# Performance work log

Measured on AMD Instinct MI355X. Metric: run time of the kernel, lower is better.

Reference implementation:

```python
import jax, jax.numpy as jnp
import numpy as np

HEADS = 8
DEPTH = 2
LN_EPS = 1e-5


def _layernorm(x, g, b):
    m = jnp.mean(x, axis=-1, keepdims=True)
    v = jnp.var(x, axis=-1, keepdims=True)
    return (x - m) / jnp.sqrt(v + LN_EPS) * g + b


def setup_inputs() -> dict:
    key = jax.random.key(0)
    ks = jax.random.split(key, 16)
    b, c, n, t = 4, 64, 512, 12
    L, H = DEPTH, 256  # depth, mlp_dim
    s = 0.05
    return {
        'x': jax.random.normal(ks[0], (b, c, n, t), jnp.float32),
        'adj': jax.random.uniform(ks[1], (n, n), jnp.float32) / n,
        'pos': 0.02 * jax.random.normal(ks[2], (1, n, c), jnp.float32),
        'qkv_w': s * jax.random.normal(ks[3], (L, 3 * c, c), jnp.float32),
        'proj_w': s * jax.random.normal(ks[4], (L, c, c), jnp.float32),
        'proj_b': jnp.zeros((L, c), jnp.float32),
        'ln_g': jnp.ones((L, c), jnp.float32),
        'ln_b': jnp.zeros((L, c), jnp.float32),
        'ff_w1': s * jax.random.normal(ks[5], (L, H, c), jnp.float32),
        'ff_b1': jnp.zeros((L, H), jnp.float32),
        'ff_w2': s * jax.random.normal(ks[6], (L, c, H), jnp.float32),
        'ff_b2': jnp.zeros((L, c), jnp.float32),
        'gcn_w': s * jax.random.normal(ks[7], (L, c, 3 * c), jnp.float32),  # Conv2d 1x1: [c_out, 3*c_in]
        'gcn_b': jnp.zeros((L, c), jnp.float32),
    }


def reference(x, adj, pos, qkv_w, proj_w, proj_b, ln_g, ln_b,
              ff_w1, ff_b1, ff_w2, ff_b2, gcn_w, gcn_b):
    b, c, n, t = x.shape
    hd = c // HEADS
    scale = hd ** (-0.5)
    # [b, c, n, t] -> [b*t, n, c]
    h = jnp.transpose(x, (0, 3, 2, 1)).reshape(b * t, n, c) + pos
    for l in range(DEPTH):
        residual = h.reshape(b, t, n, c)
        # --- manual MHA (no pre-norm around attention, faithful to source) ---
        qkv = jnp.einsum('bnc,oc->bno', h, qkv_w[l])  # [bt, n, 3c]
        qkv = qkv.reshape(b * t, n, 3, HEADS, hd).transpose(2, 0, 3, 1, 4)
        q, k, v = qkv[0], qkv[1], qkv[2]  # [bt, heads, n, hd]
        attn = jax.nn.softmax(jnp.einsum('bhnd,bhmd->bhnm', q, k) * scale, axis=-1)
        o = jnp.einsum('bhnm,bhmd->bhnd', attn, v)
        o = o.transpose(0, 2, 1, 3).reshape(b * t, n, c)
        o = jnp.einsum('bnc,oc->bno', o, proj_w[l]) + proj_b[l]
        h = o + h
        # --- PreNorm FeedForward ---
        y = _layernorm(h, ln_g[l], ln_b[l])
        y = jax.nn.gelu(jnp.einsum('bnc,hc->bnh', y, ff_w1[l]) + ff_b1[l], approximate=False)
        y = jnp.einsum('bnh,ch->bnc', y, ff_w2[l]) + ff_b2[l]
        h = y + h
        # --- GCN on residual (order=2 diffusion) ---
        r = jnp.transpose(residual, (0, 3, 2, 1))  # [b, c, n, t]
        x1 = jnp.einsum('bcvt,vw->bcwt', r, adj)
        x2 = jnp.einsum('bcvt,vw->bcwt', x1, adj)
        cat = jnp.concatenate([r, x1, x2], axis=1)  # [b, 3c, n, t]
        g = jnp.einsum('bknt,ok->bont', cat, gcn_w[l]) + gcn_b[l][None, :, None, None]
        h = jnp.transpose(g, (0, 3, 2, 1)).reshape(b * t, n, c) + h
    return jnp.transpose(h.reshape(b, t, n, c), (0, 3, 2, 1))
```

## Files before the change

### kernel.cpp

```cpp
#include <hip/hip_runtime.h>
#include <math.h>


typedef __fp16 half_t;
typedef __attribute__((ext_vector_type(2))) __fp16 half2v;
typedef __attribute__((ext_vector_type(4))) __fp16 half4v;
typedef __attribute__((ext_vector_type(4))) float f32x4;

union PU  { half2v h2[2]; half4v h4; };
union F4H { float4 f; half4v h[2]; };
union F2H { float2 f2; half4v h4; };

#define ATS 72
#define BTS 68
#define KLS 20
#define QLS 20
#define VTS 516

__global__ __launch_bounds__(256) void k_pre(const float* __restrict__ x,
                                             const float* __restrict__ pos,
                                             const float* __restrict__ adj,
                                             const float* __restrict__ qkv_w,
                                             const float* __restrict__ proj_w,
                                             const float* __restrict__ ff_w1,
                                             const float* __restrict__ ff_w2,
                                             const float* __restrict__ gcn_w,
                                             float* __restrict__ h,
                                             half_t* __restrict__ hh,
                                             half_t* __restrict__ adjTh,
                                             half_t* __restrict__ wh,
                                             half_t* __restrict__ adjT2h) {
    __shared__ __align__(16) char smem[17920];
    float* t = (float*)smem;
    int tid = threadIdx.x;
    int bidx = blockIdx.x;
    if (bidx < 384) {
        int b = bidx / 96, vt0 = (bidx % 96) * 64;
#pragma unroll
        for (int i = 0; i < 4; ++i) {
            int g = tid + i * 256;
            int r = g >> 4, q = g & 15;
            *(float4*)&t[r * 65 + 4 * q] =
                *(const float4*)(x + ((size_t)(b * 64 + r)) * 6144 + vt0 + 4 * q);
        }
        __syncthreads();
#pragma unroll
        for (int i = 0; i < 4; ++i) {
            int g = tid + i * 256;
            int r = g >> 4, q = g & 15;
            int vt = vt0 + r;
            int v = vt / 12, tt = vt - v * 12;
            float4 pv = *(const float4*)(pos + v * 64 + 4 * q);
            float4 o;
            o.x = t[(4 * q + 0) * 65 + r] + pv.x;
            o.y = t[(4 * q + 1) * 65 + r] + pv.y;
            o.z = t[(4 * q + 2) * 65 + r] + pv.z;
            o.w = t[(4 * q + 3) * 65 + r] + pv.w;
            size_t idx = ((size_t)((b * 12 + tt) * 512 + v)) * 64 + 4 * q;
            *(float4*)(h + idx) = o;
            PU u;
            u.h2[0] = __builtin_amdgcn_cvt_pkrtz(o.x, o.y);
            u.h2[1] = __builtin_amdgcn_cvt_pkrtz(o.z, o.w);
            *(half4v*)(hh + idx) = u.h4;
        }
    } else if (bidx < 448) {
        int fb = bidx - 384;
        int v0 = (fb & 7) * 64, w0 = (fb >> 3) * 64;
#pragma unroll
        for (int i = 0; i < 4; ++i) {
            int g = tid + i * 256;
            int r = g >> 4, q = g & 15;
            float4 a = *(const float4*)(adj + (size_t)(v0 + r) * 512 + w0 + 4 * q);
            t[(4 * q + 0) * 65 + r] = a.x;
            t[(4 * q + 1) * 65 + r] = a.y;
            t[(4 * q + 2) * 65 + r] = a.z;
            t[(4 * q + 3) * 65 + r] = a.w;
        }
        __syncthreads();
#pragma unroll
        for (int i = 0; i < 4; ++i) {
            int g = tid + i * 256;
            int rw = g >> 4, q = g & 15;
            const float* src = &t[rw * 65 + 4 * q];
            PU u;
            u.h2[0] = __builtin_amdgcn_cvt_pkrtz(src[0], src[1]);
            u.h2[1] = __builtin_amdgcn_cvt_pkrtz(src[2], src[3]);
            *(half4v*)(adjTh + (size_t)(w0 + rw) * 512 + v0 + 4 * q) = u.h4;
        }
    } else if (bidx < 568) {
        int i = ((bidx - 448) * 256 + tid) * 4;
        float4 v;
        if (i < 24576) v = *(const float4*)(qkv_w + i);
        else if (i < 32768) v = *(const float4*)(proj_w + (i - 24576));
        else if (i < 65536) v = *(const float4*)(ff_w1 + (i - 32768));
        else if (i < 98304) v = *(const float4*)(ff_w2 + (i - 65536));
        else v = *(const float4*)(gcn_w + (i - 98304));
        PU u;
        u.h2[0] = __builtin_amdgcn_cvt_pkrtz(v.x, v.y);
        u.h2[1] = __builtin_amdgcn_cvt_pkrtz(v.z, v.w);
        *(half4v*)(wh + i) = u.h4;
    } else {
        half_t* a_t = (half_t*)smem;
        half_t* b_t = (half_t*)smem + 64 * ATS;
        int fb = bidx - 568;
        int w0 = (fb & 7) * 64, v0 = (fb >> 3) * 64;
        int wave = tid >> 6, lane = tid & 63;
        int lm = lane & 15, lg = lane >> 4;
        const f32x4 zc = {0.f, 0.f, 0.f, 0.f};
        f32x4 acc[4] = {zc, zc, zc, zc};
        for (int kc = 0; kc < 8; ++kc) {
#pragma unroll
            for (int i = 0; i < 4; ++i) {
                int g = tid + i * 256;
                int uu = g >> 4, q = g & 15;
                float4 a = *(const float4*)(adj + (size_t)(kc * 64 + uu) * 512 + w0 + 4 * q);
                a_t[(4 * q + 0) * ATS + uu] = (half_t)a.x;
                a_t[(4 * q + 1) * ATS + uu] = (half_t)a.y;
                a_t[(4 * q + 2) * ATS + uu] = (half_t)a.z;
                a_t[(4 * q + 3) * ATS + uu] = (half_t)a.w;
            }
#pragma unroll
            for (int i = 0; i < 4; ++i) {
                int g = tid + i * 256;
                int c = g >> 4, q = g & 15;
                float4 a = *(const float4*)(adj + (size_t)(v0 + c) * 512 + kc * 64 + 4 * q);
                PU u;
                u.h2[0] = __builtin_amdgcn_cvt_pkrtz(a.x, a.y);
                u.h2[1] = __builtin_amdgcn_cvt_pkrtz(a.z, a.w);
                *(half4v*)&b_t[c * BTS + 4 * q] = u.h4;
            }
            __syncthreads();
#pragma unroll
            for (int k16 = 0; k16 < 4; ++k16) {
                half4v af = *(const half4v*)&a_t[(wave * 16 + lm) * ATS + k16 * 16 + lg * 4];
#pragma unroll
                for (int nt = 0; nt < 4; ++nt) {
                    half4v bf = *(const half4v*)&b_t[(nt * 16 + lm) * BTS + k16 * 16 + lg * 4];
                    acc[nt] = __builtin_amdgcn_mfma_f32_16x16x16f16(af, bf, acc[nt], 0, 0, 0);
                }
            }
            __syncthreads();
        }
#pragma unroll
        for (int nt = 0; nt < 4; ++nt)
#pragma unroll
            for (int r = 0; r < 4; ++r)
                adjT2h[(size_t)(w0 + wave * 16 + lg * 4 + r) * 512 + v0 + nt * 16 + lm] =
                    (half_t)acc[nt][r];
    }
}

__global__ __launch_bounds__(256) void k_qd(const half_t* __restrict__ hh,
                                            const half_t* __restrict__ Wh,
                                            half_t* __restrict__ qh,
                                            half_t* __restrict__ kh,
                                            half_t* __restrict__ vh,
                                            const half_t* __restrict__ adjTh,
                                            const half_t* __restrict__ adjT2h,
                                            half_t* __restrict__ x1h,
                                            half_t* __restrict__ x2h) {
    __shared__ __align__(16) half_t sbuf[2 * 64 * ATS + 64 * BTS];
    int tid = threadIdx.x;
    int bidx = blockIdx.x;
    int wave = tid >> 6, lane = tid & 63;
    int lm = lane & 15, lg = lane >> 4;
    const f32x4 zc = {0.f, 0.f, 0.f, 0.f};

    if (bidx < 384) {
        int wid = bidx * 4 + wave;
        int row = wid * 16 + lm;
        half4v xf[4];
#pragma unroll
        for (int kc = 0; kc < 4; ++kc) {
            F2H u;
            u.f2 = *(const float2*)(hh + (size_t)row * 64 + kc * 16 + lg * 4);
            xf[kc] = u.h4;
        }
        const float SC = 0.35355339059327373f * 1.4426950408889634f;
        int bt = row >> 9, v = row & 511;
        half4v wf[4];
#pragma unroll
        for (int kc = 0; kc < 4; ++kc)
            wf[kc] = *(const half4v*)(Wh + (size_t)lm * 64 + kc * 16 + lg * 4);
#pragma unroll
        for (int nt = 0; nt < 12; ++nt) {
            half4v cw[4];
#pragma unroll
            for (int kc = 0; kc < 4; ++kc) cw[kc] = wf[kc];
            if (nt < 11) {
#pragma unroll
                for (int kc = 0; kc < 4; ++kc)
                    wf[kc] = *(const half4v*)(Wh + (size_t)((nt + 1) * 16 + lm) * 64 + kc * 16 + lg * 4);
            }
            f32x4 acc = zc;
#pragma unroll
            for (int kc = 0; kc < 4; ++kc)
                acc = __builtin_amdgcn_mfma_f32_16x16x16f16(cw[kc], xf[kc], acc, 0, 0, 0);
            int s = nt >> 2;
            if (s == 0) { acc[0] *= SC; acc[1] *= SC; acc[2] *= SC; acc[3] *= SC; }
            int head = ((nt & 3) << 1) + (lg >> 1);
            int d0 = (lg & 1) * 4;
            PU o2;
            o2.h2[0] = __builtin_amdgcn_cvt_pkrtz(acc[0], acc[1]);
            o2.h2[1] = __builtin_amdgcn_cvt_pkrtz(acc[2], acc[3]);
            half_t* dst = (s == 0) ? qh : ((s == 1) ? kh : vh);
            *(half4v*)(dst + ((size_t)(bt * 8 + head) * 512 + v) * 8 + d0) = o2.h4;
        }
    } else {
        half_t* a_t  = sbuf;
        half_t* a2_t = sbuf + 64 * ATS;
        half_t* b_t  = sbuf + 2 * 64 * ATS;
        int fb = bidx - 384;
        int w0 = (fb & 7) * 64;
        int bt = fb >> 3;
        f32x4 acc0[4] = {zc, zc, zc, zc};
        f32x4 acc1[4] = {zc, zc, zc, zc};
        for (int kc = 0; kc < 8; ++kc) {
#pragma unroll
            for (int i = 0; i < 4; ++i) {
                int g = tid + i * 256;
                if (g < 512) {
                    int r = g >> 3, s = g & 7;
                    *(float4*)&a_t[r * ATS + s * 8] =
                        *(const float4*)(adjTh + (size_t)(w0 + r) * 512 + kc * 64 + s * 8);
                } else {
                    int g2 = g - 512;
                    int r = g2 >> 3, s = g2 & 7;
                    *(float4*)&a2_t[r * ATS + s * 8] =
                        *(const float4*)(adjT2h + (size_t)(w0 + r) * 512 + kc * 64 + s * 8);
                }
            }
#pragma unroll
            for (int i = 0; i < 2; ++i) {
                int g = tid + i * 256;
                int vr = g >> 3, s = g & 7;
                F4H u;
                u.f = *(const float4*)(hh + ((size_t)(bt * 512 + kc * 64 + vr)) * 64 + s * 8);
#pragma unroll
                for (int e = 0; e < 8; ++e)
                    b_t[(s * 8 + e) * BTS + vr] = u.h[e >> 2][e & 3];
            }
            __syncthreads();
#pragma unroll
            for (int k16 = 0; k16 < 4; ++k16) {
                half4v af0 = *(const half4v*)&a_t[(wave * 16 + lm) * ATS + k16 * 16 + lg * 4];
                half4v af1 = *(const half4v*)&a2_t[(wave * 16 + lm) * ATS + k16 * 16 + lg * 4];
#pragma unroll
                for (int nt = 0; nt < 4; ++nt) {
                    half4v bf = *(const half4v*)&b_t[(nt * 16 + lm) * BTS + k16 * 16 + lg * 4];
                    acc0[nt] = __builtin_amdgcn_mfma_f32_16x16x16f16(af0, bf, acc0[nt], 0, 0, 0);
                    acc1[nt] = __builtin_amdgcn_mfma_f32_16x16x16f16(af1, bf, acc1[nt], 0, 0, 0);
                }
            }
            __syncthreads();
        }
#pragma unroll
        for (int nt = 0; nt < 4; ++nt)
#pragma unroll
            for (int r = 0; r < 4; ++r) {
                size_t o = (size_t)(w0 + wave * 16 + lg * 4 + r) * 3072 + bt * 64 + nt * 16 + lm;
                x1h[o] = (half_t)acc0[nt][r];
                x2h[o] = (half_t)acc1[nt][r];
            }
    }
}

__global__ __launch_bounds__(512) void k_ag(const half_t* __restrict__ qh,
                                            const half_t* __restrict__ kh,
                                            const half_t* __restrict__ vh,
                                            half_t* __restrict__ obh,
                                            const half_t* __restrict__ hh,
                                            const half_t* __restrict__ x1h,
                                            const half_t* __restrict__ x2h,
                                            const half_t* __restrict__ Wh,
                                            const float* __restrict__ bias,
                                            float* __restrict__ gout) {
    __shared__ __align__(16) half_t sbuf[512 * KLS + 16 * VTS + 256 * QLS];
    int tid = threadIdx.x;
    int bidx = blockIdx.x;
    const half4v zero4 = {(__fp16)0.f, (__fp16)0.f, (__fp16)0.f, (__fp16)0.f};
    const f32x4 zc = {0.f, 0.f, 0.f, 0.f};

    if (bidx < 768) {
        half_t* kl = sbuf;
        half_t* vt = sbuf + 512 * KLS;
        half_t* ql = sbuf + 512 * KLS + 16 * VTS;
        int bh = bidx >> 1;
        int half_ = bidx & 1;
        const half_t* kbase = kh + (size_t)bh * 4096;
        const half_t* vbase = vh + (size_t)bh * 4096;
        const half_t* qbase = qh + (size_t)bh * 4096 + half_ * 2048;

        if (tid < 256) {
#pragma unroll
            for (int kk = 0; kk < 2; ++kk) {
                int key = tid * 2 + kk;
                F4H u;
                u.f = *(const float4*)(kbase + key * 8);
                half4v* rowp = (half4v*)&kl[key * KLS];
                rowp[0] = u.h[0];
                rowp[1] = u.h[1];
                rowp[2] = zero4;
                rowp[3] = zero4;
            }
            {
                F4H u;
                u.f = *(const float4*)(qbase + tid * 8);
                half4v* rowp = (half4v*)&ql[tid * QLS];
                rowp[0] = u.h[0];
                rowp[1] = u.h[1];
                rowp[2] = zero4;
                rowp[3] = zero4;
            }
            {
                int k0 = tid * 2;
                F4H a, b;
                a.f = *(const float4*)(vbase + k0 * 8);
                b.f = *(const float4*)(vbase + k0 * 8 + 8);
#pragma unroll
                for (int d = 0; d < 8; ++d) {
                    half2v p = {a.h[d >> 2][d & 3], b.h[d >> 2][d & 3]};
                    *(half2v*)&vt[d * VTS + k0] = p;
                }
            }
        }
        for (int i = tid; i < 1032; i += 512)
            ((half4v*)(vt + 8 * VTS))[i] = zero4;
        __syncthreads();

        int wave = tid >> 6, lane = tid & 63;
        int lm = lane & 15, lg = lane >> 4;
        int bt = bh >> 3, head = bh & 7;

#pragma unroll 1
        for (int st = 0; st < 2; ++st) {
            int qrow0 = wave * 32 + st * 16;
            half4v qf = *(const half4v*)&ql[(qrow0 + lm) * QLS + lg * 4];
            f32x4 acc = zc;
            float l0 = 0.f, l1 = 0.f, l2 = 0.f, l3 = 0.f;
#pragma unroll 4
            for (int kt = 0; kt < 32; ++kt) {
                int key0 = kt * 16;
                half4v ka = *(const half4v*)&kl[(key0 + lm) * KLS + lg * 4];
                f32x4 c1 = __builtin_amdgcn_mfma_f32_16x16x16f16(ka, qf, zc, 0, 0, 0);
                float p0 = exp2f(fminf(c1[0], 12.f));
                float p1 = exp2f(fminf(c1[1], 12.f));
                float p2 = exp2f(fminf(c1[2], 12.f));
                float p3 = exp2f(fminf(c1[3], 12.f));
                l0 += p0; l1 += p1; l2 += p2; l3 += p3;
                PU pu;
                pu.h2[0] = __builtin_amdgcn_cvt_pkrtz(p0, p1);
                pu.h2[1] = __builtin_amdgcn_cvt_pkrtz(p2, p3);
                half4v va = *(const half4v*)&vt[lm * VTS + key0 + lg * 4];
                acc = __builtin_amdgcn_mfma_f32_16x16x16f16(va, pu.h4, acc, 0, 0, 0);
            }
            float lsum = (l0 + l1) + (l2 + l3);
            lsum += __shfl_xor(lsum, 16);
            lsum += __shfl_xor(lsum, 32);
            if (lg < 2) {
                float inv = 1.f / lsum;
                int rowg = half_ * 256 + qrow0 + lm;
                PU o2;
                o2.h2[0] = __builtin_amdgcn_cvt_pkrtz(acc[0] * inv, acc[1] * inv);
                o2.h2[1] = __builtin_amdgcn_cvt_pkrtz(acc[2] * inv, acc[3] * inv);
                *(half4v*)(obh + ((size_t)(bt * 512 + rowg)) * 64 + head * 8 + lg * 4) = o2.h4;
            }
        }
    } else {
        half_t* a_t = sbuf;
        half_t* b_t = sbuf + 64 * ATS;
        int row0 = (bidx - 768) * 64;
        int wave = tid >> 6, lane = tid & 63;
        int lm = lane & 15, lg = lane >> 4;
        int wr = wave & 3;
        int wn = wave >> 2;
        f32x4 acc[2] = {zc, zc};

        for (int ch = 0; ch < 3; ++ch) {
            {
                int g = tid;
                int r = g >> 3, s = g & 7;
                if (ch == 0) {
                    int rowg = row0 + r;
                    int v = rowg / 48, bt = rowg - v * 48;
                    *(float4*)&a_t[r * ATS + s * 8] =
                        *(const float4*)(hh + ((size_t)(bt * 512 + v)) * 64 + s * 8);
                } else {
                    const half_t* X = (ch == 1) ? x1h : x2h;
                    *(float4*)&a_t[r * ATS + s * 8] =
                        *(const float4*)(X + (size_t)(row0 + r) * 64 + s * 8);
                }
            }
#pragma unroll
            for (int i = 0; i < 2; ++i) {
                int g = tid + i * 512;
                int r = g >> 4, q = g & 15;
                *(half4v*)&b_t[r * BTS + 4 * q] =
                    *(const half4v*)(Wh + (size_t)r * 192 + ch * 64 + 4 * q);
            }
            __syncthreads();
#pragma unroll
            for (int k16 = 0; k16 < 4; ++k16) {
                half4v af = *(const half4v*)&a_t[(wr * 16 + lm) * ATS + k16 * 16 + lg * 4];
#pragma unroll
                for (int j = 0; j < 2; ++j) {
                    int nt = wn * 2 + j;
                    half4v bf = *(const half4v*)&b_t[(nt * 16 + lm) * BTS + k16 * 16 + lg * 4];
                    acc[j] = __builtin_amdgcn_mfma_f32_16x16x16f16(bf, af, acc[j], 0, 0, 0);
                }
            }
            __syncthreads();
        }
        {
            int row = row0 + wr * 16 + lm;
            int v = row / 48, bt = row - v * 48;
            float* gp = gout + ((size_t)(bt * 512 + v)) * 64;
#pragma unroll
            for (int j = 0; j < 2; ++j) {
                int nt = wn * 2 + j;
                float4 bb = *(const float4*)(bias + nt * 16 + lg * 4);
                *(float4*)(gp + nt * 16 + lg * 4) =
                    make_float4(acc[j][0] + bb.x, acc[j][1] + bb.y,
                                acc[j][2] + bb.z, acc[j][3] + bb.w);
            }
        }
    }
}

__global__ __launch_bounds__(128) void k_plf(const half_t* __restrict__ obh,
                                             const half_t* __restrict__ pwh,
                                             const float* __restrict__ pb,
                                             const float* __restrict__ g,
                                             const float* __restrict__ bln,
                                             const half_t* __restrict__ w1h,
                                             const float* __restrict__ b1,
                                             const half_t* __restrict__ w2h,
                                             const float* __restrict__ b2,
                                             const float* __restrict__ gout,
                                             float* __restrict__ h,
                                             half_t* __restrict__ hh,
                                             float* __restrict__ out,
                                             int last) {
    int wid = blockIdx.x * 2 + (threadIdx.x >> 6);
    int lane = threadIdx.x & 63;
    int lm = lane & 15, lg = lane >> 4;
    int row = wid * 16 + lm;
    const f32x4 zc = {0.f, 0.f, 0.f, 0.f};

    half4v pf[4];
#pragma unroll
    for (int kc = 0; kc < 4; ++kc)
        pf[kc] = *(const half4v*)(pwh + (size_t)lm * 64 + kc * 16 + lg * 4);

    half4v of[4];
#pragma unroll
    for (int kc = 0; kc < 4; ++kc) {
        F2H u;
        u.f2 = *(const float2*)(obh + (size_t)row * 64 + kc * 16 + lg * 4);
        of[kc] = u.h4;
    }

    f32x4 hp[4];
#pragma unroll
    for (int nt = 0; nt < 4; ++nt) {
        half4v cw[4];
#pragma unroll
        for (int kc = 0; kc < 4; ++kc) cw[kc] = pf[kc];
        if (nt < 3) {
#pragma unroll
            for (int kc = 0; kc < 4; ++kc)
                pf[kc] = *(const half4v*)(pwh + (size_t)((nt + 1) * 16 + lm) * 64 + kc * 16 + lg * 4);
        }
        f32x4 c = zc;
#pragma unroll
        for (int kc = 0; kc < 4; ++kc)
            c = __builtin_amdgcn_mfma_f32_16x16x16f16(cw[kc], of[kc], c, 0, 0, 0);
        float4 ho = *(const float4*)(h + (size_t)row * 64 + nt * 16 + lg * 4);
        float4 bb = *(const float4*)(pb + nt * 16 + lg * 4);
        hp[nt][0] = c[0] + ho.x + bb.x;
        hp[nt][1] = c[1] + ho.y + bb.y;
        hp[nt][2] = c[2] + ho.z + bb.z;
        hp[nt][3] = c[3] + ho.w + bb.w;
    }

    float s = 0.f, s2 = 0.f;
#pragma unroll
    for (int nt = 0; nt < 4; ++nt)
#pragma unroll
        for (int r = 0; r < 4; ++r) {
            s += hp[nt][r];
            s2 += hp[nt][r] * hp[nt][r];
        }
    s += __shfl_xor(s, 16);  s2 += __shfl_xor(s2, 16);
    s += __shfl_xor(s, 32);  s2 += __shfl_xor(s2, 32);
    float mean = s * (1.f / 64.f);
    float var = s2 * (1.f / 64.f) - mean * mean;
    float rstd = rsqrtf(var + 1e-5f);

    half4v xf[4];
#pragma unroll
    for (int nt = 0; nt < 4; ++nt) {
        float4 gg = *(const float4*)(g + nt * 16 + lg * 4);
        float4 bb = *(const float4*)(bln + nt * 16 + lg * 4);
        float y0 = (hp[nt][0] - mean) * rstd * gg.x + bb.x;
        float y1 = (hp[nt][1] - mean) * rstd * gg.y + bb.y;
        float y2 = (hp[nt][2] - mean) * rstd * gg.z + bb.z;
        float y3 = (hp[nt][3] - mean) * rstd * gg.w + bb.w;
        PU u;
        u.h2[0] = __builtin_amdgcn_cvt_pkrtz(y0, y1);
        u.h2[1] = __builtin_amdgcn_cvt_pkrtz(y2, y3);
        xf[nt] = u.h4;
    }

    half4v w1f[4];
#pragma unroll
    for (int kc = 0; kc < 4; ++kc)
        w1f[kc] = *(const half4v*)(w1h + (size_t)lm * 64 + kc * 16 + lg * 4);

    f32x4 acc[4] = {zc, zc, zc, zc};
#pragma unroll 4
    for (int ht = 0; ht < 16; ++ht) {
        half4v cw[4];
#pragma unroll
        for (int kc = 0; kc < 4; ++kc) cw[kc] = w1f[kc];
        half4v w2f[4];
#pragma unroll
        for (int ot = 0; ot < 4; ++ot)
            w2f[ot] = *(const half4v*)(w2h + (size_t)(ot * 16 + lm) * 256 + ht * 16 + lg * 4);
        if (ht < 15) {
#pragma unroll
            for (int kc = 0; kc < 4; ++kc)
                w1f[kc] = *(const half4v*)(w1h + (size_t)((ht + 1) * 16 + lm) * 64 + kc * 16 + lg * 4);
        }
        f32x4 c1 = zc;
#pragma unroll
        for (int kc = 0; kc < 4; ++kc)
            c1 = __builtin_amdgcn_mfma_f32_16x16x16f16(cw[kc], xf[kc], c1, 0, 0, 0);
        float4 bb = *(const float4*)(b1 + ht * 16 + lg * 4);
        float y0 = c1[0] + bb.x;
        float y1 = c1[1] + bb.y;
        float y2 = c1[2] + bb.z;
        float y3 = c1[3] + bb.w;
        y0 = 0.5f * y0 * (1.0f + erff(y0 * 0.70710678118654752f));
        y1 = 0.5f * y1 * (1.0f + erff(y1 * 0.70710678118654752f));
        y2 = 0.5f * y2 * (1.0f + erff(y2 * 0.70710678118654752f));
        y3 = 0.5f * y3 * (1.0f + erff(y3 * 0.70710678118654752f));
        PU p;
        p.h2[0] = __builtin_amdgcn_cvt_pkrtz(y0, y1);
        p.h2[1] = __builtin_amdgcn_cvt_pkrtz(y2, y3);
#pragma unroll
        for (int ot = 0; ot < 4; ++ot)
            acc[ot] = __builtin_amdgcn_mfma_f32_16x16x16f16(w2f[ot], p.h4, acc[ot], 0, 0, 0);
    }

    if (!last) {
#pragma unroll
        for (int ot = 0; ot < 4; ++ot) {
            float4 bb = *(const float4*)(b2 + ot * 16 + lg * 4);
            float4 gv = *(const float4*)(gout + (size_t)row * 64 + ot * 16 + lg * 4);
            float4 fv = make_float4(hp[ot][0] + acc[ot][0] + bb.x + gv.x,
                                    hp[ot][1] + acc[ot][1] + bb.y + gv.y,
                                    hp[ot][2] + acc[ot][2] + bb.z + gv.z,
                                    hp[ot][3] + acc[ot][3] + bb.w + gv.w);
            size_t idx = (size_t)row * 64 + ot * 16 + lg * 4;
            *(float4*)(h + idx) = fv;
            PU u;
            u.h2[0] = __builtin_amdgcn_cvt_pkrtz(fv.x, fv.y);
            u.h2[1] = __builtin_amdgcn_cvt_pkrtz(fv.z, fv.w);
            *(half4v*)(hh + idx) = u.h4;
        }
    } else {
        int bt = row >> 9, v = row & 511;
        int b = bt / 12, t = bt - b * 12;
        float* op = out + (size_t)b * 393216 + v * 12 + t;
#pragma unroll
        for (int ot = 0; ot < 4; ++ot) {
            float4 bb = *(const float4*)(b2 + ot * 16 + lg * 4);
            float4 gv = *(const float4*)(gout + (size_t)row * 64 + ot * 16 + lg * 4);
            int c0 = ot * 16 + lg * 4;
            op[(size_t)(c0 + 0) * 6144] = hp[ot][0] + acc[ot][0] + bb.x + gv.x;
            op[(size_t)(c0 + 1) * 6144] = hp[ot][1] + acc[ot][1] + bb.y + gv.y;
            op[(size_t)(c0 + 2) * 6144] = hp[ot][2] + acc[ot][2] + bb.z + gv.z;
            op[(size_t)(c0 + 3) * 6144] = hp[ot][3] + acc[ot][3] + bb.w + gv.w;
        }
    }
}

extern "C" void kernel_launch(void* const* d_in, const int* in_sizes, int n_in,
                              void* d_out, int out_size, void* d_ws, size_t ws_size,
                              hipStream_t stream) {
    const float* x      = (const float*)d_in[0];
    const float* adj    = (const float*)d_in[1];
    const float* pos    = (const float*)d_in[2];
    const float* qkv_w  = (const float*)d_in[3];
    const float* proj_w = (const float*)d_in[4];
    const float* proj_b = (const float*)d_in[5];
    const float* ln_g   = (const float*)d_in[6];
    const float* ln_b   = (const float*)d_in[7];
    const float* ff_w1  = (const float*)d_in[8];
    const float* ff_b1  = (const float*)d_in[9];
    const float* ff_w2  = (const float*)d_in[10];
    const float* ff_b2  = (const float*)d_in[11];
    const float* gcn_w  = (const float*)d_in[12];
    const float* gcn_b  = (const float*)d_in[13];
    float* out = (float*)d_out;

    const size_t SZ = 1572864;
    float* h    = (float*)d_ws;
    float* gout = h + SZ;
    half_t* hh  = (half_t*)(gout + SZ);
    half_t* x1h = hh + SZ;
    half_t* x2h = x1h + SZ;
    half_t* qh  = x2h + SZ;
    half_t* kh  = qh + SZ;
    half_t* vh  = kh + SZ;
    half_t* obh = vh + SZ;
    half_t* adjTh  = obh + SZ;
    half_t* adjT2h = adjTh + 262144;
    half_t* wh     = adjT2h + 262144;
    half_t* qkv_wh  = wh;
    half_t* proj_wh = wh + 24576;
    half_t* ff_w1h  = wh + 32768;
    half_t* ff_w2h  = wh + 65536;
    half_t* gcn_wh  = wh + 98304;

    k_pre<<<632, 256, 0, stream>>>(x, pos, adj, qkv_w, proj_w, ff_w1, ff_w2, gcn_w,
                                   h, hh, adjTh, wh, adjT2h);
    for (int l = 0; l < 2; ++l) {
        k_qd<<<768, 256, 0, stream>>>(hh, qkv_wh + l * 12288, qh, kh, vh,
                                      adjTh, adjT2h, x1h, x2h);
        k_ag<<<1152, 512, 0, stream>>>(qh, kh, vh, obh, hh, x1h, x2h,
                                       gcn_wh + l * 12288, gcn_b + l * 64, gout);
        k_plf<<<768, 128, 0, stream>>>(obh, proj_wh + l * 4096, proj_b + l * 64,
                                       ln_g + l * 64, ln_b + l * 64,
                                       ff_w1h + l * 16384, ff_b1 + l * 256,
                                       ff_w2h + l * 16384, ff_b2 + l * 64, gout, h, hh,
                                       out, l);
    }
}
```

Baseline: 276.7 us.

## Shrink attention LDS with register zero-padding and coalesce GCN diffusion stores

In the attention path, K, Q and V are now stored in LDS unpadded. The zero padding the MFMA needs is supplied by selecting zero vectors in registers based on the lane index. This removes the padding writes and roughly halves LDS usage, which may allow more blocks to be resident. In the diffusion kernel, results are staged through LDS and written with 16-byte vector stores instead of scattered 2-byte stores. The cost is an extra barrier and some extra select instructions inside the inner loop.

```diff
diff --git a/kernel.cpp b/kernel.cpp
--- a/kernel.cpp
+++ b/kernel.cpp
@@ -13,8 +13,6 @@
 
 #define ATS 72
 #define BTS 68
-#define KLS 20
-#define QLS 20
 #define VTS 516
 
 __global__ __launch_bounds__(256) void k_pre(const float* __restrict__ x,
@@ -254,14 +252,25 @@
             }
             __syncthreads();
         }
+        half_t* x1s = sbuf;
+        half_t* x2s = sbuf + 64 * 72;
 #pragma unroll
         for (int nt = 0; nt < 4; ++nt)
 #pragma unroll
             for (int r = 0; r < 4; ++r) {
-                size_t o = (size_t)(w0 + wave * 16 + lg * 4 + r) * 3072 + bt * 64 + nt * 16 + lm;
-                x1h[o] = (half_t)acc0[nt][r];
-                x2h[o] = (half_t)acc1[nt][r];
-            }
+                int vrow = wave * 16 + lg * 4 + r;
+                x1s[vrow * 72 + nt * 16 + lm] = (half_t)acc0[nt][r];
+                x2s[vrow * 72 + nt * 16 + lm] = (half_t)acc1[nt][r];
+            }
+        __syncthreads();
+#pragma unroll
+        for (int i = 0; i < 2; ++i) {
+            int g = tid + i * 256;
+            int r = g >> 3, s = g & 7;
+            size_t o = (size_t)(w0 + r) * 3072 + bt * 64 + s * 8;
+            *(float4*)(x1h + o) = *(const float4*)&x1s[r * 72 + s * 8];
+            *(float4*)(x2h + o) = *(const float4*)&x2s[r * 72 + s * 8];
+        }
     }
 }
 
@@ -275,7 +284,7 @@
                                             const half_t* __restrict__ Wh,
                                             const float* __restrict__ bias,
                                             float* __restrict__ gout) {
-    __shared__ __align__(16) half_t sbuf[512 * KLS + 16 * VTS + 256 * QLS];
+    __shared__ __align__(16) half_t sbuf[10272];
     int tid = threadIdx.x;
     int bidx = blockIdx.x;
     const half4v zero4 = {(__fp16)0.f, (__fp16)0.f, (__fp16)0.f, (__fp16)0.f};
@@ -283,8 +292,8 @@
 
     if (bidx < 768) {
         half_t* kl = sbuf;
-        half_t* vt = sbuf + 512 * KLS;
-        half_t* ql = sbuf + 512 * KLS + 16 * VTS;
+        half_t* vt = sbuf + 4096;
+        half_t* ql = sbuf + 4096 + 8 * VTS;
         int bh = bidx >> 1;
         int half_ = bidx & 1;
         const half_t* kbase = kh + (size_t)bh * 4096;
@@ -292,26 +301,9 @@
         const half_t* qbase = qh + (size_t)bh * 4096 + half_ * 2048;
 
         if (tid < 256) {
-#pragma unroll
-            for (int kk = 0; kk < 2; ++kk) {
-                int key = tid * 2 + kk;
-                F4H u;
-                u.f = *(const float4*)(kbase + key * 8);
-                half4v* rowp = (half4v*)&kl[key * KLS];
-                rowp[0] = u.h[0];
-                rowp[1] = u.h[1];
-                rowp[2] = zero4;
-                rowp[3] = zero4;
-            }
-            {
-                F4H u;
-                u.f = *(const float4*)(qbase + tid * 8);
-                half4v* rowp = (half4v*)&ql[tid * QLS];
-                rowp[0] = u.h[0];
-                rowp[1] = u.h[1];
-                rowp[2] = zero4;
-                rowp[3] = zero4;
-            }
+            *(float4*)&kl[tid * 16]     = *(const float4*)(kbase + tid * 16);
+            *(float4*)&kl[tid * 16 + 8] = *(const float4*)(kbase + tid * 16 + 8);
+            *(float4*)&ql[tid * 8]      = *(const float4*)(qbase + tid * 8);
             {
                 int k0 = tid * 2;
                 F4H a, b;
@@ -324,8 +316,6 @@
                 }
             }
         }
-        for (int i = tid; i < 1032; i += 512)
-            ((half4v*)(vt + 8 * VTS))[i] = zero4;
         __syncthreads();
 
         int wave = tid >> 6, lane = tid & 63;
@@ -335,13 +325,15 @@
 #pragma unroll 1
         for (int st = 0; st < 2; ++st) {
             int qrow0 = wave * 32 + st * 16;
-            half4v qf = *(const half4v*)&ql[(qrow0 + lm) * QLS + lg * 4];
+            half4v qt = *(const half4v*)&ql[(qrow0 + lm) * 8 + (lg & 1) * 4];
+            half4v qf = (lg < 2) ? qt : zero4;
             f32x4 acc = zc;
             float l0 = 0.f, l1 = 0.f, l2 = 0.f, l3 = 0.f;
 #pragma unroll 4
             for (int kt = 0; kt < 32; ++kt) {
                 int key0 = kt * 16;
-                half4v ka = *(const half4v*)&kl[(key0 + lm) * KLS + lg * 4];
+                half4v kt_ = *(const half4v*)&kl[(key0 + lm) * 8 + (lg & 1) * 4];
+                half4v ka = (lg < 2) ? kt_ : zero4;
                 f32x4 c1 = __builtin_amdgcn_mfma_f32_16x16x16f16(ka, qf, zc, 0, 0, 0);
                 float p0 = exp2f(fminf(c1[0], 12.f));
                 float p1 = exp2f(fminf(c1[1], 12.f));
@@ -351,7 +343,8 @@
                 PU pu;
                 pu.h2[0] = __builtin_amdgcn_cvt_pkrtz(p0, p1);
                 pu.h2[1] = __builtin_amdgcn_cvt_pkrtz(p2, p3);
-                half4v va = *(const half4v*)&vt[lm * VTS + key0 + lg * 4];
+                half4v vv = *(const half4v*)&vt[(lm & 7) * VTS + key0 + lg * 4];
+                half4v va = (lm < 8) ? vv : zero4;
                 acc = __builtin_amdgcn_mfma_f32_16x16x16f16(va, pu.h4, acc, 0, 0, 0);
             }
             float lsum = (l0 + l1) + (l2 + l3);
```

Measured after the change: 283.5 us. 2.5% more time.
